# Optimization experiments

Hardware: AMD Instinct MI355X
Metric: run time of the kernel (lower is better)

## Reference

```python
import jax, jax.numpy as jnp
import numpy as np

C_DIM = 256


def setup_inputs() -> dict:
    key = jax.random.key(0)
    k_x, k_g, k_w1, k_b1, k_w2, k_b2 = jax.random.split(key, 6)
    B, C, H, W = 16, C_DIM, 96, 96
    r = C // 8
    x = jax.random.normal(k_x, (B, C, H, W), dtype=jnp.float32)
    gamma = jax.random.normal(k_g, (1,), dtype=jnp.float32) * 0.1
    # SE excitation MLP: Linear(C -> C//8), ReLU, Linear(C//8 -> C), Sigmoid
    w1 = jax.random.normal(k_w1, (r, C), dtype=jnp.float32) * (1.0 / np.sqrt(C))
    b1 = jax.random.normal(k_b1, (r,), dtype=jnp.float32) * 0.01
    w2 = jax.random.normal(k_w2, (C, r), dtype=jnp.float32) * (1.0 / np.sqrt(r))
    b2 = jax.random.normal(k_b2, (C,), dtype=jnp.float32) * 0.01
    return {"x": x, "gamma": gamma, "w1": w1, "b1": b1, "w2": w2, "b2": b2}


def reference(x, gamma, w1, b1, w2, b2):
    B, C, H, W = x.shape
    v = x.reshape(B, C, H * W)                       # proj_query == proj_value
    # channel-channel energy: [B, C, C]
    energy = jnp.einsum("bcn,bdn->bcd", v, v)
    energy_new = jnp.max(energy, axis=-1, keepdims=True) - energy
    attention = jax.nn.softmax(energy_new, axis=-1)
    ch_out = jnp.einsum("bcd,bdn->bcn", attention, v).reshape(B, C, H, W)
    # SE branch: global avg pool -> MLP -> sigmoid gate per (b, c)
    pooled = jnp.mean(x, axis=(2, 3))                # [B, C]
    hidden = jax.nn.relu(pooled @ w1.T + b1)         # [B, C//8]
    gate = jax.nn.sigmoid(hidden @ w2.T + b2)        # [B, C]
    # per-(b,c) scale (vectorized form of the B*C python loop) + residual
    out = gamma * (ch_out * gate[:, :, None, None]) + x
    return out
```

## Files before the change

### kernel.cpp

```cpp
#include <hip/hip_runtime.h>
#include <math.h>

#define BATCH 16
#define CDIM 256
#define HW 9216
#define RDIM 32
#define SPLITS 16
#define KSLAB (HW / SPLITS)
#define KCH 32
#define NCH (KSLAB / KCH)

#define BN 64
#define BK 64
#define VOFF 32768

typedef __attribute__((ext_vector_type(8))) short short8;
typedef __attribute__((ext_vector_type(4))) short short4_t;
typedef __attribute__((ext_vector_type(4))) float f32x4;
typedef __attribute__((ext_vector_type(8))) _Float16 half8;

__device__ __forceinline__ unsigned short bf16_rne(float x) {
    union { float f; unsigned u; } a; a.f = x;
    return (unsigned short)((a.u + 0x7fffu + ((a.u >> 16) & 1u)) >> 16);
}
__device__ __forceinline__ unsigned pack2(float lo, float hi) {
    return (unsigned)bf16_rne(lo) | ((unsigned)bf16_rne(hi) << 16);
}

__device__ __forceinline__ void lds_barrier() {
    asm volatile("s_waitcnt lgkmcnt(0)" ::: "memory");
    __builtin_amdgcn_s_barrier();
}

__device__ __forceinline__ void gload16(const void* g, void* l) {
    __builtin_amdgcn_global_load_lds(
        (const __attribute__((address_space(1))) unsigned*)g,
        (__attribute__((address_space(3))) unsigned*)l, 16, 0, 0);
}

__device__ __forceinline__ int gswz16(int row, int k) {
    int byte = (row << 6) + (k << 1);
    byte ^= (((row >> 1) ^ (row >> 3)) & 3) << 4;
    return byte >> 1;
}
__device__ __forceinline__ int bofs(int row, int k) {
    return (((row) << 7) | ((k) << 1)) ^ (((row ^ (row >> 2)) & 7) << 4);
}

template <bool ATOMIC>
__global__ __launch_bounds__(1024) void gram_kernel(const float* __restrict__ x,
                                                    float* __restrict__ part,
                                                    float* __restrict__ pooled) {
    int split = blockIdx.x;
    int b     = blockIdx.y;
    const float* v = x + (size_t)b * CDIM * HW;
    int kbase0 = split * KSLAB;

    __shared__ _Float16 lds[2][CDIM * KCH];

    int t    = threadIdx.x;
    int row  = t >> 2;
    int kq   = t & 3;
    int lane = t & 63;
    int wave = t >> 6;
    int wr   = wave >> 2, wc = wave & 3;
    int lhi  = lane >> 4, llo = lane & 15;

    const float4* vrow = (const float4*)(v + (size_t)row * HW);

    f32x4 acc[4][4];
    #pragma unroll
    for (int i = 0; i < 4; ++i)
        #pragma unroll
        for (int j = 0; j < 4; ++j)
            acc[i][j] = (f32x4){0.f, 0.f, 0.f, 0.f};

    float psum = 0.f;
    float4 fa0, fa1, fb0, fb1;

    {
        int kb0 = kbase0;
        fa0 = vrow[(kb0 >> 2) + kq * 2];
        fa1 = vrow[(kb0 >> 2) + kq * 2 + 1];
        int kb1 = kbase0 + KCH;
        fb0 = vrow[(kb1 >> 2) + kq * 2];
        fb1 = vrow[(kb1 >> 2) + kq * 2 + 1];
    }

    auto body = [&](float4& g0, float4& g1, _Float16* buf, int ch) {
        float vals[8] = { g0.x, g0.y, g0.z, g0.w, g1.x, g1.y, g1.z, g1.w };
        half8 h;
        #pragma unroll
        for (int j = 0; j < 8; ++j) {
            psum += vals[j];
            h[j] = (_Float16)vals[j];
        }
        *(half8*)&buf[gswz16(row, kq * 8)] = h;
        if (ch + 2 < NCH) {
            int kb = kbase0 + (ch + 2) * KCH;
            g0 = vrow[(kb >> 2) + kq * 2];
            g1 = vrow[(kb >> 2) + kq * 2 + 1];
        }
        lds_barrier();

        half8 A[4], B[4];
        #pragma unroll
        for (int rb = 0; rb < 4; ++rb)
            A[rb] = *(const half8*)&buf[gswz16(wr * 64 + rb * 16 + llo, lhi * 8)];
        #pragma unroll
        for (int cb = 0; cb < 4; ++cb)
            B[cb] = *(const half8*)&buf[gswz16(wc * 64 + cb * 16 + llo, lhi * 8)];

        __builtin_amdgcn_s_setprio(1);
        #pragma unroll
        for (int rb = 0; rb < 4; ++rb)
            #pragma unroll
            for (int cb = 0; cb < 4; ++cb)
                acc[rb][cb] = __builtin_amdgcn_mfma_f32_16x16x32_f16(A[rb], B[cb], acc[rb][cb], 0, 0, 0);
        __builtin_amdgcn_s_setprio(0);
    };

    #pragma unroll 1
    for (int it = 0; it < NCH / 2; ++it) {
        body(fa0, fa1, (_Float16*)lds[0], it * 2);
        body(fb0, fb1, (_Float16*)lds[1], it * 2 + 1);
    }

    psum += __shfl_xor(psum, 1);
    psum += __shfl_xor(psum, 2);
    if (kq == 0) atomicAdd(&pooled[b * CDIM + row], psum);

    if (ATOMIC) {
        #pragma unroll
        for (int rb = 0; rb < 4; ++rb) {
            int r0 = wr * 64 + rb * 16 + lhi * 4;
            #pragma unroll
            for (int cb = 0; cb < 4; ++cb) {
                int c0 = wc * 64 + cb * 16 + llo;
                #pragma unroll
                for (int reg = 0; reg < 4; ++reg)
                    atomicAdd(&part[((size_t)b * CDIM + r0 + reg) * CDIM + c0], acc[rb][cb][reg]);
            }
        }
    } else {
        float* pb = part + ((size_t)split * BATCH + b) * CDIM * CDIM;
        #pragma unroll
        for (int rb = 0; rb < 4; ++rb) {
            int r0 = wr * 64 + rb * 16 + lhi * 4;
            #pragma unroll
            for (int cb = 0; cb < 4; ++cb) {
                int c0 = wc * 64 + cb * 16 + llo;
                #pragma unroll
                for (int reg = 0; reg < 4; ++reg)
                    __builtin_nontemporal_store(acc[rb][cb][reg],
                        &pb[(size_t)(r0 + reg) * CDIM + c0]);
            }
        }
    }
}

__global__ __launch_bounds__(256) void se_kernel(const float* __restrict__ pooled,
                                                 const float* __restrict__ w1,
                                                 const float* __restrict__ b1,
                                                 const float* __restrict__ w2,
                                                 const float* __restrict__ b2,
                                                 float* __restrict__ gate) {
    int b = blockIdx.x;
    int t = threadIdx.x;
    __shared__ float p[CDIM];
    __shared__ float hid[RDIM];
    p[t] = pooled[b * CDIM + t] * (1.0f / HW);
    __syncthreads();
    if (t < RDIM) {
        float s = b1[t];
        const float* wr = w1 + t * CDIM;
        for (int k = 0; k < CDIM; ++k) s = fmaf(wr[k], p[k], s);
        hid[t] = s > 0.f ? s : 0.f;
    }
    __syncthreads();
    float s = b2[t];
    const float* wr = w2 + t * RDIM;
    #pragma unroll
    for (int k = 0; k < RDIM; ++k) s = fmaf(wr[k], hid[k], s);
    gate[b * CDIM + t] = 1.0f / (1.0f + expf(-s));
}

__global__ __launch_bounds__(256) void softmax_kernel(const float* __restrict__ part,
                                                      unsigned short* __restrict__ atts) {
    int row = blockIdx.x;
    int b = row >> 8, c = row & 255;
    int t = threadIdx.x;
    const float* p0 = part + (size_t)row * CDIM + t;
    float val = 0.f;
    #pragma unroll
    for (int s = 0; s < SPLITS; ++s)
        val += __builtin_nontemporal_load(&p0[(size_t)s * BATCH * CDIM * CDIM]);

    float m = val;
    for (int off = 32; off > 0; off >>= 1) m = fminf(m, __shfl_down(m, off));
    __shared__ float redm[4];
    if ((t & 63) == 0) redm[t >> 6] = m;
    __syncthreads();
    float rowmin = fminf(fminf(redm[0], redm[1]), fminf(redm[2], redm[3]));

    float p = expf(rowmin - val);
    float s = p;
    for (int off = 32; off > 0; off >>= 1) s += __shfl_down(s, off);
    __shared__ float reds[4];
    if ((t & 63) == 0) reds[t >> 6] = s;
    __syncthreads();
    float tot = reds[0] + reds[1] + reds[2] + reds[3];

    size_t idx = (size_t)b * 65536 + (size_t)(t >> 6) * 16384 + (bofs(c, t & 63) >> 1);
    atts[idx] = bf16_rne(p / tot);
}

__global__ __launch_bounds__(256) void softmax1_kernel(const float* __restrict__ energy,
                                                       unsigned short* __restrict__ atts) {
    int row = blockIdx.x;
    int b = row >> 8, c = row & 255;
    int t = threadIdx.x;
    float val = energy[(size_t)row * CDIM + t];

    float m = val;
    for (int off = 32; off > 0; off >>= 1) m = fminf(m, __shfl_down(m, off));
    __shared__ float redm[4];
    if ((t & 63) == 0) redm[t >> 6] = m;
    __syncthreads();
    float rowmin = fminf(fminf(redm[0], redm[1]), fminf(redm[2], redm[3]));

    float p = expf(rowmin - val);
    float s = p;
    for (int off = 32; off > 0; off >>= 1) s += __shfl_down(s, off);
    __shared__ float reds[4];
    if ((t & 63) == 0) reds[t >> 6] = s;
    __syncthreads();
    float tot = reds[0] + reds[1] + reds[2] + reds[3];

    size_t idx = (size_t)b * 65536 + (size_t)(t >> 6) * 16384 + (bofs(c, t & 63) >> 1);
    atts[idx] = bf16_rne(p / tot);
}

__global__ __launch_bounds__(256, 4) void out_kernel(const unsigned short* __restrict__ atts,
                                                     const float* __restrict__ x,
                                                     const float* __restrict__ gate,
                                                     const float* __restrict__ gammap,
                                                     float* __restrict__ out) {
    __shared__ __align__(16) char lds[40960];

    const int t    = threadIdx.x;
    const int lane = t & 63;
    const int wave = t >> 6;
    const int lhi  = lane >> 4, llo = lane & 15;
    const int nblk = blockIdx.x * BN;
    const int b    = blockIdx.y;

    const float* v     = x + (size_t)b * CDIM * HW;
    const char*  attsB = (const char*)atts + (size_t)b * 131072;

    f32x4 acc[4][4];
    #pragma unroll
    for (int i = 0; i < 4; ++i)
        #pragma unroll
        for (int j = 0; j < 4; ++j)
            acc[i][j] = (f32x4){0.f, 0.f, 0.f, 0.f};

    const int ddp = t >> 3;
    const int n8  = (t & 7) * 8;
    float4 vr0a, vr0b, vr1a, vr1b;

    auto load_v = [&](int k0) {
        const float* r0 = v + (size_t)(k0 + 2 * ddp) * HW + nblk + n8;
        vr0a = *(const float4*)r0;
        vr0b = *(const float4*)(r0 + 4);
        vr1a = *(const float4*)(r0 + HW);
        vr1b = *(const float4*)(r0 + HW + 4);
    };

    load_v(0);

    for (int ch = 0; ch < 4; ++ch) {
        __syncthreads();
        #pragma unroll
        for (int i = 0; i < 8; ++i)
            gload16(attsB + ch * 32768 + i * 4096 + t * 16, lds + i * 4096 + t * 16);
        {
            const float* f0a = (const float*)&vr0a;
            const float* f0b = (const float*)&vr0b;
            const float* f1a = (const float*)&vr1a;
            const float* f1b = (const float*)&vr1b;
            #pragma unroll
            for (int j = 0; j < 4; ++j) {
                *(unsigned*)(lds + VOFF + bofs(n8 + j,     2 * ddp)) = pack2(f0a[j], f1a[j]);
                *(unsigned*)(lds + VOFF + bofs(n8 + 4 + j, 2 * ddp)) = pack2(f0b[j], f1b[j]);
            }
        }
        __syncthreads();

        if (ch < 3) load_v((ch + 1) * BK);

        #pragma unroll
        for (int ks = 0; ks < 2; ++ks) {
            int kb = ks * 32 + lhi * 8;
            short8 An[4], Bc[4];
            #pragma unroll
            for (int rb = 0; rb < 4; ++rb)
                An[rb] = *(const short8*)(lds + VOFF + bofs(rb * 16 + llo, kb));
            #pragma unroll
            for (int cb = 0; cb < 4; ++cb)
                Bc[cb] = *(const short8*)(lds + bofs(wave * 64 + cb * 16 + llo, kb));
            #pragma unroll
            for (int rb = 0; rb < 4; ++rb)
                #pragma unroll
                for (int cb = 0; cb < 4; ++cb)
                    acc[rb][cb] = __builtin_amdgcn_mfma_f32_16x16x32_bf16(An[rb], Bc[cb], acc[rb][cb], 0, 0, 0);
        }
    }

    float gm = gammap[0];
    float gv[4];
    #pragma unroll
    for (int cb = 0; cb < 4; ++cb)
        gv[cb] = gm * gate[b * CDIM + wave * 64 + cb * 16 + llo];

    #pragma unroll
    for (int rb = 0; rb < 4; ++rb) {
        int n0 = rb * 16 + lhi * 4;
        #pragma unroll
        for (int cb = 0; cb < 4; ++cb) {
            int c = wave * 64 + cb * 16 + llo;
            size_t base = ((size_t)b * CDIM + c) * HW + nblk + n0;
            f32x4 xv = *(const f32x4*)&x[base];
            f32x4 o;
            o[0] = fmaf(acc[rb][cb][0], gv[cb], xv[0]);
            o[1] = fmaf(acc[rb][cb][1], gv[cb], xv[1]);
            o[2] = fmaf(acc[rb][cb][2], gv[cb], xv[2]);
            o[3] = fmaf(acc[rb][cb][3], gv[cb], xv[3]);
            __builtin_nontemporal_store(o, (f32x4*)&out[base]);
        }
    }
}

extern "C" void kernel_launch(void* const* d_in, const int* in_sizes, int n_in,
                              void* d_out, int out_size, void* d_ws, size_t ws_size,
                              hipStream_t stream) {
    const float* x     = (const float*)d_in[0];
    const float* gamma = (const float*)d_in[1];
    const float* w1    = (const float*)d_in[2];
    const float* b1    = (const float*)d_in[3];
    const float* w2    = (const float*)d_in[4];
    const float* b2    = (const float*)d_in[5];
    float* out = (float*)d_out;

    const size_t ee        = (size_t)BATCH * CDIM * CDIM;
    const size_t partElems = (size_t)SPLITS * ee;
    const size_t needPart  = partElems * sizeof(float) + ee * 2 + 2 * BATCH * CDIM * sizeof(float);

    if (ws_size >= needPart) {
        float*          part   = (float*)d_ws;
        unsigned short* atts   = (unsigned short*)(part + partElems);
        float*          pooled = (float*)(atts + ee);
        float*          gate   = pooled + BATCH * CDIM;

        hipMemsetAsync(pooled, 0, (size_t)BATCH * CDIM * sizeof(float), stream);
        gram_kernel<false><<<dim3(SPLITS, BATCH), 1024, 0, stream>>>(x, part, pooled);
        se_kernel<<<BATCH, 256, 0, stream>>>(pooled, w1, b1, w2, b2, gate);
        softmax_kernel<<<BATCH * CDIM, 256, 0, stream>>>(part, atts);
        out_kernel<<<dim3(HW / BN, BATCH), 256, 0, stream>>>(atts, x, gate, gamma, out);
    } else {
        float*          energy = (float*)d_ws;
        unsigned short* atts   = (unsigned short*)(energy + ee);
        float*          pooled = (float*)(atts + ee);
        float*          gate   = pooled + BATCH * CDIM;

        hipMemsetAsync(energy, 0, ee * sizeof(float), stream);
        hipMemsetAsync(pooled, 0, (size_t)BATCH * CDIM * sizeof(float), stream);
        gram_kernel<true><<<dim3(SPLITS, BATCH), 1024, 0, stream>>>(x, energy, pooled);
        se_kernel<<<BATCH, 256, 0, stream>>>(pooled, w1, b1, w2, b2, gate);
        softmax1_kernel<<<BATCH * CDIM, 256, 0, stream>>>(energy, atts);
        out_kernel<<<dim3(HW / BN, BATCH), 256, 0, stream>>>(atts, x, gate, gamma, out);
    }
}
```

Baseline: 170.2 us.

## Load attention fragments directly into registers and double-buffer V tile in LDS

The out kernel stops staging the full 32KB attention chunk through LDS via global_load_lds and instead loads each wave's attention fragments straight from global memory into registers. The bf16 V tile is double-buffered in a smaller 16KB LDS region, so one barrier per chunk replaces two. MFMA sections are wrapped in s_setprio to favor matrix issue. The aim is lower LDS footprint (higher occupancy) and fewer barriers, at the cost of more scattered global reads for the attention operand.

```diff
diff --git a/kernel.cpp b/kernel.cpp
--- a/kernel.cpp
+++ b/kernel.cpp
@@ -12,7 +12,6 @@
 
 #define BN 64
 #define BK 64
-#define VOFF 32768
 
 typedef __attribute__((ext_vector_type(8))) short short8;
 typedef __attribute__((ext_vector_type(4))) short short4_t;
@@ -30,12 +29,6 @@
 __device__ __forceinline__ void lds_barrier() {
     asm volatile("s_waitcnt lgkmcnt(0)" ::: "memory");
     __builtin_amdgcn_s_barrier();
-}
-
-__device__ __forceinline__ void gload16(const void* g, void* l) {
-    __builtin_amdgcn_global_load_lds(
-        (const __attribute__((address_space(1))) unsigned*)g,
-        (__attribute__((address_space(3))) unsigned*)l, 16, 0, 0);
 }
 
 __device__ __forceinline__ int gswz16(int row, int k) {
@@ -246,7 +239,7 @@
                                                      const float* __restrict__ gate,
                                                      const float* __restrict__ gammap,
                                                      float* __restrict__ out) {
-    __shared__ __align__(16) char lds[40960];
+    __shared__ __align__(16) char lds[16384];
 
     const int t    = threadIdx.x;
     const int lane = t & 63;
@@ -280,10 +273,7 @@
     load_v(0);
 
     for (int ch = 0; ch < 4; ++ch) {
-        __syncthreads();
-        #pragma unroll
-        for (int i = 0; i < 8; ++i)
-            gload16(attsB + ch * 32768 + i * 4096 + t * 16, lds + i * 4096 + t * 16);
+        char* buf = lds + (ch & 1) * 8192;
         {
             const float* f0a = (const float*)&vr0a;
             const float* f0b = (const float*)&vr0b;
@@ -291,29 +281,36 @@
             const float* f1b = (const float*)&vr1b;
             #pragma unroll
             for (int j = 0; j < 4; ++j) {
-                *(unsigned*)(lds + VOFF + bofs(n8 + j,     2 * ddp)) = pack2(f0a[j], f1a[j]);
-                *(unsigned*)(lds + VOFF + bofs(n8 + 4 + j, 2 * ddp)) = pack2(f0b[j], f1b[j]);
+                *(unsigned*)(buf + bofs(n8 + j,     2 * ddp)) = pack2(f0a[j], f1a[j]);
+                *(unsigned*)(buf + bofs(n8 + 4 + j, 2 * ddp)) = pack2(f0b[j], f1b[j]);
             }
         }
-        __syncthreads();
-
+        short8 Bc0[4], Bc1[4];
+        #pragma unroll
+        for (int cb = 0; cb < 4; ++cb) {
+            int c = wave * 64 + cb * 16 + llo;
+            Bc0[cb] = *(const short8*)(attsB + ch * 32768 + bofs(c, lhi * 8));
+            Bc1[cb] = *(const short8*)(attsB + ch * 32768 + bofs(c, 32 + lhi * 8));
+        }
         if (ch < 3) load_v((ch + 1) * BK);
+
+        lds_barrier();
 
         #pragma unroll
         for (int ks = 0; ks < 2; ++ks) {
             int kb = ks * 32 + lhi * 8;
-            short8 An[4], Bc[4];
+            short8 An[4];
             #pragma unroll
             for (int rb = 0; rb < 4; ++rb)
-                An[rb] = *(const short8*)(lds + VOFF + bofs(rb * 16 + llo, kb));
-            #pragma unroll
-            for (int cb = 0; cb < 4; ++cb)
-                Bc[cb] = *(const short8*)(lds + bofs(wave * 64 + cb * 16 + llo, kb));
+                An[rb] = *(const short8*)(buf + bofs(rb * 16 + llo, kb));
+            __builtin_amdgcn_s_setprio(1);
             #pragma unroll
             for (int rb = 0; rb < 4; ++rb)
                 #pragma unroll
                 for (int cb = 0; cb < 4; ++cb)
-                    acc[rb][cb] = __builtin_amdgcn_mfma_f32_16x16x32_bf16(An[rb], Bc[cb], acc[rb][cb], 0, 0, 0);
+                    acc[rb][cb] = __builtin_amdgcn_mfma_f32_16x16x32_bf16(
+                        An[rb], ks ? Bc1[cb] : Bc0[cb], acc[rb][cb], 0, 0, 0);
+            __builtin_amdgcn_s_setprio(0);
         }
     }
 
```

After: 245.5 us. +44.2%, slower.

## Store split-K Gram partials as fp16 and shrink out_kernel attention LDS tiles

Applied to the files above, without the earlier changes.

Gram partial sums are now written as fp16 in a quad-row interleaved layout instead of fp32, which halves the partial-buffer write and read traffic. The softmax kernel now handles four rows per block with vectorized half4 loads, and writes attention in a new 32-wide swizzled layout. out_kernel streams attention in 32-column K slices with a smaller LDS buffer, which may allow higher occupancy. Storing the partial sums in fp16 loses some precision, and the sums could overflow if energies grow large.

```diff
diff --git a/kernel.cpp b/kernel.cpp
--- a/kernel.cpp
+++ b/kernel.cpp
@@ -11,13 +11,13 @@
 #define NCH (KSLAB / KCH)
 
 #define BN 64
-#define BK 64
-#define VOFF 32768
+#define VOFF 16384
 
 typedef __attribute__((ext_vector_type(8))) short short8;
 typedef __attribute__((ext_vector_type(4))) short short4_t;
 typedef __attribute__((ext_vector_type(4))) float f32x4;
 typedef __attribute__((ext_vector_type(8))) _Float16 half8;
+typedef __attribute__((ext_vector_type(4))) _Float16 half4;
 
 __device__ __forceinline__ unsigned short bf16_rne(float x) {
     union { float f; unsigned u; } a; a.f = x;
@@ -46,10 +46,16 @@
 __device__ __forceinline__ int bofs(int row, int k) {
     return (((row) << 7) | ((k) << 1)) ^ (((row ^ (row >> 2)) & 7) << 4);
 }
+__device__ __forceinline__ int aofs(int row, int k) {
+    int byte = (row << 6) + (k << 1);
+    byte ^= (((row >> 1) ^ (row >> 3)) & 3) << 4;
+    return byte;
+}
 
 template <bool ATOMIC>
 __global__ __launch_bounds__(1024) void gram_kernel(const float* __restrict__ x,
-                                                    float* __restrict__ part,
+                                                    float* __restrict__ energyA,
+                                                    _Float16* __restrict__ part16,
                                                     float* __restrict__ pooled) {
     int split = blockIdx.x;
     int b     = blockIdx.y;
@@ -139,21 +145,24 @@
                 int c0 = wc * 64 + cb * 16 + llo;
                 #pragma unroll
                 for (int reg = 0; reg < 4; ++reg)
-                    atomicAdd(&part[((size_t)b * CDIM + r0 + reg) * CDIM + c0], acc[rb][cb][reg]);
+                    atomicAdd(&energyA[((size_t)b * CDIM + r0 + reg) * CDIM + c0], acc[rb][cb][reg]);
             }
         }
     } else {
-        float* pb = part + ((size_t)split * BATCH + b) * CDIM * CDIM;
+        _Float16* pb = part16 + ((size_t)split * BATCH + b) * CDIM * CDIM;
         #pragma unroll
         for (int rb = 0; rb < 4; ++rb) {
-            int r0 = wr * 64 + rb * 16 + lhi * 4;
+            int rq = wr * 16 + rb * 4 + lhi;
             #pragma unroll
             for (int cb = 0; cb < 4; ++cb) {
-                int c0 = wc * 64 + cb * 16 + llo;
-                #pragma unroll
-                for (int reg = 0; reg < 4; ++reg)
-                    __builtin_nontemporal_store(acc[rb][cb][reg],
-                        &pb[(size_t)(r0 + reg) * CDIM + c0]);
+                int d = wc * 64 + cb * 16 + llo;
+                half4 hv;
+                hv[0] = (_Float16)acc[rb][cb][0];
+                hv[1] = (_Float16)acc[rb][cb][1];
+                hv[2] = (_Float16)acc[rb][cb][2];
+                hv[3] = (_Float16)acc[rb][cb][3];
+                __builtin_nontemporal_store(hv,
+                    (half4*)(pb + ((size_t)rq * CDIM + d) * 4));
             }
         }
     }
@@ -185,34 +194,50 @@
     gate[b * CDIM + t] = 1.0f / (1.0f + expf(-s));
 }
 
-__global__ __launch_bounds__(256) void softmax_kernel(const float* __restrict__ part,
+__global__ __launch_bounds__(256) void softmax_kernel(const _Float16* __restrict__ part16,
                                                       unsigned short* __restrict__ atts) {
-    int row = blockIdx.x;
-    int b = row >> 8, c = row & 255;
+    int blk = blockIdx.x;
+    int b = blk >> 6, cq = blk & 63;
     int t = threadIdx.x;
-    const float* p0 = part + (size_t)row * CDIM + t;
-    float val = 0.f;
-    #pragma unroll
-    for (int s = 0; s < SPLITS; ++s)
-        val += __builtin_nontemporal_load(&p0[(size_t)s * BATCH * CDIM * CDIM]);
-
-    float m = val;
-    for (int off = 32; off > 0; off >>= 1) m = fminf(m, __shfl_down(m, off));
-    __shared__ float redm[4];
-    if ((t & 63) == 0) redm[t >> 6] = m;
-    __syncthreads();
-    float rowmin = fminf(fminf(redm[0], redm[1]), fminf(redm[2], redm[3]));
-
-    float p = expf(rowmin - val);
-    float s = p;
-    for (int off = 32; off > 0; off >>= 1) s += __shfl_down(s, off);
-    __shared__ float reds[4];
-    if ((t & 63) == 0) reds[t >> 6] = s;
-    __syncthreads();
-    float tot = reds[0] + reds[1] + reds[2] + reds[3];
-
-    size_t idx = (size_t)b * 65536 + (size_t)(t >> 6) * 16384 + (bofs(c, t & 63) >> 1);
-    atts[idx] = bf16_rne(p / tot);
+    int lane = t & 63, w = t >> 6;
+
+    float val[4] = {0.f, 0.f, 0.f, 0.f};
+    const _Float16* p0 = part16 + ((size_t)cq * CDIM + t) * 4;
+    #pragma unroll
+    for (int s = 0; s < SPLITS; ++s) {
+        half4 hv = __builtin_nontemporal_load(
+            (const half4*)(p0 + ((size_t)(s * BATCH + b)) * CDIM * CDIM));
+        val[0] += (float)hv[0];
+        val[1] += (float)hv[1];
+        val[2] += (float)hv[2];
+        val[3] += (float)hv[3];
+    }
+
+    __shared__ float redm[4][4], reds[4][4];
+    #pragma unroll
+    for (int j = 0; j < 4; ++j) {
+        float m = val[j];
+        for (int off = 32; off > 0; off >>= 1) m = fminf(m, __shfl_down(m, off));
+        if (lane == 0) redm[j][w] = m;
+    }
+    __syncthreads();
+    float p[4];
+    #pragma unroll
+    for (int j = 0; j < 4; ++j) {
+        float rowmin = fminf(fminf(redm[j][0], redm[j][1]), fminf(redm[j][2], redm[j][3]));
+        p[j] = expf(rowmin - val[j]);
+        float s = p[j];
+        for (int off = 32; off > 0; off >>= 1) s += __shfl_down(s, off);
+        if (lane == 0) reds[j][w] = s;
+    }
+    __syncthreads();
+    #pragma unroll
+    for (int j = 0; j < 4; ++j) {
+        float tot = reds[j][0] + reds[j][1] + reds[j][2] + reds[j][3];
+        int c = cq * 4 + j;
+        size_t idx = (size_t)b * 131072 + (size_t)(t >> 5) * 16384 + aofs(c, t & 31);
+        *(unsigned short*)((char*)atts + idx) = bf16_rne(p[j] / tot);
+    }
 }
 
 __global__ __launch_bounds__(256) void softmax1_kernel(const float* __restrict__ energy,
@@ -237,8 +262,8 @@
     __syncthreads();
     float tot = reds[0] + reds[1] + reds[2] + reds[3];
 
-    size_t idx = (size_t)b * 65536 + (size_t)(t >> 6) * 16384 + (bofs(c, t & 63) >> 1);
-    atts[idx] = bf16_rne(p / tot);
+    size_t idx = (size_t)b * 131072 + (size_t)(t >> 5) * 16384 + aofs(c, t & 31);
+    *(unsigned short*)((char*)atts + idx) = bf16_rne(p / tot);
 }
 
 __global__ __launch_bounds__(256, 4) void out_kernel(const unsigned short* __restrict__ atts,
@@ -246,7 +271,7 @@
                                                      const float* __restrict__ gate,
                                                      const float* __restrict__ gammap,
                                                      float* __restrict__ out) {
-    __shared__ __align__(16) char lds[40960];
+    __shared__ __align__(16) char lds[24576];
 
     const int t    = threadIdx.x;
     const int lane = t & 63;
@@ -279,12 +304,12 @@
 
     load_v(0);
 
-    for (int ch = 0; ch < 4; ++ch) {
+    for (int kh = 0; kh < 8; ++kh) {
         __syncthreads();
         #pragma unroll
-        for (int i = 0; i < 8; ++i)
-            gload16(attsB + ch * 32768 + i * 4096 + t * 16, lds + i * 4096 + t * 16);
-        {
+        for (int i = 0; i < 4; ++i)
+            gload16(attsB + kh * 16384 + i * 4096 + t * 16, lds + i * 4096 + t * 16);
+        if ((kh & 1) == 0) {
             const float* f0a = (const float*)&vr0a;
             const float* f0b = (const float*)&vr0b;
             const float* f1a = (const float*)&vr1a;
@@ -297,18 +322,17 @@
         }
         __syncthreads();
 
-        if (ch < 3) load_v((ch + 1) * BK);
-
-        #pragma unroll
-        for (int ks = 0; ks < 2; ++ks) {
-            int kb = ks * 32 + lhi * 8;
+        if (kh < 7 && (kh & 1) == 1) load_v((kh + 1) * 32);
+
+        {
+            int kb = (kh & 1) * 32 + lhi * 8;
             short8 An[4], Bc[4];
             #pragma unroll
             for (int rb = 0; rb < 4; ++rb)
                 An[rb] = *(const short8*)(lds + VOFF + bofs(rb * 16 + llo, kb));
             #pragma unroll
             for (int cb = 0; cb < 4; ++cb)
-                Bc[cb] = *(const short8*)(lds + bofs(wave * 64 + cb * 16 + llo, kb));
+                Bc[cb] = *(const short8*)(lds + aofs(wave * 64 + cb * 16 + llo, lhi * 8));
             #pragma unroll
             for (int rb = 0; rb < 4; ++rb)
                 #pragma unroll
@@ -352,20 +376,20 @@
     const float* b2    = (const float*)d_in[5];
     float* out = (float*)d_out;
 
-    const size_t ee        = (size_t)BATCH * CDIM * CDIM;
-    const size_t partElems = (size_t)SPLITS * ee;
-    const size_t needPart  = partElems * sizeof(float) + ee * 2 + 2 * BATCH * CDIM * sizeof(float);
+    const size_t ee       = (size_t)BATCH * CDIM * CDIM;
+    const size_t partHalf = (size_t)SPLITS * ee;
+    const size_t needPart = partHalf * 2 + ee * 2 + 2 * BATCH * CDIM * sizeof(float);
 
     if (ws_size >= needPart) {
-        float*          part   = (float*)d_ws;
-        unsigned short* atts   = (unsigned short*)(part + partElems);
+        _Float16*       part16 = (_Float16*)d_ws;
+        unsigned short* atts   = (unsigned short*)(part16 + partHalf);
         float*          pooled = (float*)(atts + ee);
         float*          gate   = pooled + BATCH * CDIM;
 
         hipMemsetAsync(pooled, 0, (size_t)BATCH * CDIM * sizeof(float), stream);
-        gram_kernel<false><<<dim3(SPLITS, BATCH), 1024, 0, stream>>>(x, part, pooled);
+        gram_kernel<false><<<dim3(SPLITS, BATCH), 1024, 0, stream>>>(x, nullptr, part16, pooled);
         se_kernel<<<BATCH, 256, 0, stream>>>(pooled, w1, b1, w2, b2, gate);
-        softmax_kernel<<<BATCH * CDIM, 256, 0, stream>>>(part, atts);
+        softmax_kernel<<<BATCH * 64, 256, 0, stream>>>(part16, atts);
         out_kernel<<<dim3(HW / BN, BATCH), 256, 0, stream>>>(atts, x, gate, gamma, out);
     } else {
         float*          energy = (float*)d_ws;
@@ -375,7 +399,7 @@
 
         hipMemsetAsync(energy, 0, ee * sizeof(float), stream);
         hipMemsetAsync(pooled, 0, (size_t)BATCH * CDIM * sizeof(float), stream);
-        gram_kernel<true><<<dim3(SPLITS, BATCH), 1024, 0, stream>>>(x, energy, pooled);
+        gram_kernel<true><<<dim3(SPLITS, BATCH), 1024, 0, stream>>>(x, energy, nullptr, pooled);
         se_kernel<<<BATCH, 256, 0, stream>>>(pooled, w1, b1, w2, b2, gate);
         softmax1_kernel<<<BATCH * CDIM, 256, 0, stream>>>(energy, atts);
         out_kernel<<<dim3(HW / BN, BATCH), 256, 0, stream>>>(atts, x, gate, gamma, out);
```

Measured after the change: 151.0 us. 11.3% less time.
